# Kernel tuning notes

Hardware: AMD Instinct MI355X
Metric: run time of the kernel (lower is better)

The kernel has to match this reference:

```python
import jax, jax.numpy as jnp
import numpy as np


def setup_inputs() -> dict:
    key = jax.random.key(0)
    k1, k2 = jax.random.split(key)
    pred_corners = jax.random.normal(k1, (2048, 8, 3), dtype=jnp.float32)
    gt_corners = jax.random.normal(k2, (2048, 8, 3), dtype=jnp.float32)
    return {"pred_corners": pred_corners, "gt_corners": gt_corners}


def _chamfer(pred_corners, gt_corners):
    # flatten boxes -> point clouds: [Np*8, 3], [Ng*8, 3]
    x = pred_corners.reshape(-1, 3)
    y = gt_corners.reshape(-1, 3)
    x2 = jnp.sum(x * x, axis=-1)  # [N]
    y2 = jnp.sum(y * y, axis=-1)  # [M]
    d2 = x2[:, None] + y2[None, :] - 2.0 * jnp.einsum("nd,md->nm", x, y)
    dist = jnp.sqrt(jnp.maximum(d2, 0.0))  # [N, M]
    # bidirectional min, averaged per box (8 corners) then over boxes
    min_p2g = jnp.min(dist, axis=1).reshape(-1, 8).mean(axis=1)
    min_g2p = jnp.min(dist, axis=0).reshape(-1, 8).mean(axis=1)
    return min_p2g.mean() + min_g2p.mean()


def reference(pred_corners, gt_corners):
    return _chamfer(pred_corners, gt_corners)
```

## Files before the change

kernel.cpp:

```cpp
#include <hip/hip_runtime.h>


#define NPTS   16384
#define RPT    8
#define BLOCK  256
#define XPB    (RPT * BLOCK)
#define NXB    (NPTS / XPB)
#define NSEG   128
#define YSEG   (NPTS / NSEG)
#define CHUNK  32
#define CPAD   257
#define WS_NEED (2 * NPTS * 4)

__global__ __launch_bounds__(BLOCK, 4) void chamfer_both(
        const float* __restrict__ pred, const float* __restrict__ gt,
        unsigned int* __restrict__ minp, unsigned int* __restrict__ ming) {
    const int xb  = blockIdx.x;
    const int ys  = blockIdx.y;
    const int tid = threadIdx.x;

    __shared__ float4 shy[YSEG];
    __shared__ float  shp[CHUNK * CPAD];

    if (tid < YSEG) {
        int yi = ys * YSEG + tid;
        float a = gt[3 * yi + 0], b = gt[3 * yi + 1], c = gt[3 * yi + 2];
        shy[tid] = make_float4(a, b, c, -0.5f * (a * a + b * b + c * c));
    }

    float xx[RPT], xy[RPT], xz[RPT], x2[RPT], hv[RPT], rmx[RPT];
    const int xbase = xb * XPB;
#pragma unroll
    for (int r = 0; r < RPT; ++r) {
        int xi = xbase + r * BLOCK + tid;
        xx[r] = pred[3 * xi + 0];
        xy[r] = pred[3 * xi + 1];
        xz[r] = pred[3 * xi + 2];
        x2[r] = xx[r] * xx[r] + xy[r] * xy[r] + xz[r] * xz[r];
        hv[r] = 0.5f * x2[r];
        rmx[r] = -3.0e38f;
    }

    __syncthreads();

    for (int c = 0; c < YSEG; c += CHUNK) {
#pragma unroll 2
        for (int jj = 0; jj < CHUNK; jj += 2) {
            float4 y0 = shy[c + jj];
            float4 y1 = shy[c + jj + 1];
            float u0[RPT], u1[RPT];
#pragma unroll
            for (int r = 0; r < RPT; ++r) {
                float t0 = fmaf(xz[r], y0.z, y0.w);
                t0 = fmaf(xy[r], y0.y, t0);
                t0 = fmaf(xx[r], y0.x, t0);
                float t1 = fmaf(xz[r], y1.z, y1.w);
                t1 = fmaf(xy[r], y1.y, t1);
                t1 = fmaf(xx[r], y1.x, t1);
                rmx[r] = fmaxf(rmx[r], fmaxf(t0, t1));
                u0[r] = t0 - hv[r];
                u1[r] = t1 - hv[r];
            }
            float g0 = fmaxf(fmaxf(fmaxf(u0[0], u0[1]), u0[2]),
                             fmaxf(fmaxf(u0[3], u0[4]), u0[5]));
            float cp0 = fmaxf(fmaxf(g0, u0[6]), u0[7]);
            float g1 = fmaxf(fmaxf(fmaxf(u1[0], u1[1]), u1[2]),
                             fmaxf(fmaxf(u1[3], u1[4]), u1[5]));
            float cp1 = fmaxf(fmaxf(g1, u1[6]), u1[7]);
            shp[(jj + 0) * CPAD + tid] = cp0;
            shp[(jj + 1) * CPAD + tid] = cp1;
        }
        __syncthreads();
        {
            const int jl = tid >> 3;
            const int sl = tid & 7;
            float m = -3.0e38f;
#pragma unroll 8
            for (int k = 0; k < 32; ++k)
                m = fmaxf(m, shp[jl * CPAD + sl + 8 * k]);
            m = fmaxf(m, __shfl_xor(m, 1, 64));
            m = fmaxf(m, __shfl_xor(m, 2, 64));
            m = fmaxf(m, __shfl_xor(m, 4, 64));
            if (sl == 0) {
                int yj = ys * YSEG + c + jl;
                float d2 = fmaxf(-2.0f * m, 0.0f);
                atomicMin(&ming[yj], __float_as_uint(d2));
            }
        }
        __syncthreads();
    }

#pragma unroll
    for (int r = 0; r < RPT; ++r) {
        int xi = xbase + r * BLOCK + tid;
        float d2 = fmaxf(fmaf(-2.0f, rmx[r], x2[r]), 0.0f);
        atomicMin(&minp[xi], __float_as_uint(d2));
    }
}

__global__ __launch_bounds__(256) void chamfer_reduce(
        const unsigned int* __restrict__ mins, float* __restrict__ out) {
    const int gid = blockIdx.x * 256 + threadIdx.x;
    float s = 0.0f;
#pragma unroll
    for (int i = 0; i < 2; ++i)
        s += sqrtf(__uint_as_float(mins[gid + i * 64 * 256]));
#pragma unroll
    for (int off = 32; off > 0; off >>= 1)
        s += __shfl_down(s, off, 64);
    if ((threadIdx.x & 63) == 0)
        atomicAdd(out, s * (1.0f / (float)NPTS));
}


__global__ __launch_bounds__(256) void init_mins(unsigned int* mins, float* out) {
    int i = blockIdx.x * blockDim.x + threadIdx.x;
    if (i < 2 * NPTS) mins[i] = 0x7F800000u;
    if (i == 0) out[0] = 0.0f;
}

__global__ __launch_bounds__(BLOCK, 4) void chamfer_min_atomic(
        const float* __restrict__ pred, const float* __restrict__ gt,
        unsigned int* __restrict__ mins) {
    const int xb  = blockIdx.x;
    const int ys  = blockIdx.y;
    const int dir = blockIdx.z;
    const float* __restrict__ X = dir ? gt : pred;
    const float* __restrict__ Y = dir ? pred : gt;
    unsigned int* __restrict__ outm = mins + dir * NPTS;
    const int tid = threadIdx.x;

    __shared__ float4 sh[YSEG];
    if (tid < YSEG) {
        int yi = ys * YSEG + tid;
        float a = Y[3 * yi + 0], b = Y[3 * yi + 1], c = Y[3 * yi + 2];
        sh[tid] = make_float4(a, b, c, -0.5f * (a * a + b * b + c * c));
    }
    float xx[RPT], xy[RPT], xz[RPT], x2[RPT], mx[RPT];
    const int xbase = xb * XPB;
#pragma unroll
    for (int r = 0; r < RPT; ++r) {
        int xi = xbase + r * BLOCK + tid;
        xx[r] = X[3 * xi + 0];
        xy[r] = X[3 * xi + 1];
        xz[r] = X[3 * xi + 2];
        x2[r] = xx[r] * xx[r] + xy[r] * xy[r] + xz[r] * xz[r];
        mx[r] = -3.0e38f;
    }
    __syncthreads();
#pragma unroll 2
    for (int j = 0; j < YSEG; j += 2) {
        float4 y0 = sh[j], y1 = sh[j + 1];
#pragma unroll
        for (int r = 0; r < RPT; ++r) {
            float t0 = fmaf(xz[r], y0.z, y0.w);
            t0 = fmaf(xy[r], y0.y, t0);
            t0 = fmaf(xx[r], y0.x, t0);
            float t1 = fmaf(xz[r], y1.z, y1.w);
            t1 = fmaf(xy[r], y1.y, t1);
            t1 = fmaf(xx[r], y1.x, t1);
            mx[r] = fmaxf(mx[r], fmaxf(t0, t1));
        }
    }
#pragma unroll
    for (int r = 0; r < RPT; ++r) {
        int xi = xbase + r * BLOCK + tid;
        float d2 = fmaxf(fmaf(-2.0f, mx[r], x2[r]), 0.0f);
        atomicMin(&outm[xi], __float_as_uint(d2));
    }
}

extern "C" void kernel_launch(void* const* d_in, const int* in_sizes, int n_in,
                              void* d_out, int out_size, void* d_ws, size_t ws_size,
                              hipStream_t stream) {
    const float* pred = (const float*)d_in[0];
    const float* gt   = (const float*)d_in[1];
    float* out        = (float*)d_out;
    unsigned int* minp = (unsigned int*)d_ws;
    unsigned int* ming = minp + NPTS;

    if (ws_size >= (size_t)WS_NEED) {
        hipMemsetAsync(d_ws, 0xFF, (size_t)WS_NEED, stream);
        hipMemsetAsync(d_out, 0, sizeof(float), stream);
        hipLaunchKernelGGL(chamfer_both, dim3(NXB, NSEG), dim3(BLOCK), 0, stream,
                           pred, gt, minp, ming);
        hipLaunchKernelGGL(chamfer_reduce, dim3(64), dim3(256), 0, stream,
                           minp, out);
    } else {
        hipLaunchKernelGGL(init_mins, dim3((2 * NPTS + 255) / 256), dim3(256), 0,
                           stream, minp, out);
        hipLaunchKernelGGL(chamfer_min_atomic, dim3(NXB, NSEG, 2), dim3(BLOCK), 0,
                           stream, pred, gt, minp);
        hipLaunchKernelGGL(chamfer_reduce, dim3(64), dim3(256), 0, stream,
                           minp, out);
    }
}
```

Measured before the change: 103.3 us.

## Compute pairwise distance tiles with bf16 split-precision MFMA instead of scalar FMAs

Replaces the scalar-FMA chamfer kernel with one that encodes each point as hi/lo bf16 parts plus the half-norm term, so a single 32x32x16 bf16 MFMA yields the full x·y - |x|²/2 - |y|²/2 tile. Row minima are kept in registers and reduced with shuffles, while column minima go through LDS atomics before one global atomic per column. The aim is to move the O(N·M) arithmetic onto the matrix cores. In exchange it accepts bf16 split rounding error and many LDS atomics per tile.

Measured after the change: 102.1 us. No clear change (-1.1%).

```diff
diff --git a/kernel.cpp b/kernel.cpp
--- a/kernel.cpp
+++ b/kernel.cpp
@@ -2,99 +2,137 @@
 
 
 #define NPTS   16384
-#define RPT    8
-#define BLOCK  256
-#define XPB    (RPT * BLOCK)
-#define NXB    (NPTS / XPB)
-#define NSEG   128
-#define YSEG   (NPTS / NSEG)
-#define CHUNK  32
-#define CPAD   257
+#define YS     1024
+#define NYS    (NPTS / YS)
+#define NXG    (NPTS / 128)
+#define ONEBF  0x3F80u
 #define WS_NEED (2 * NPTS * 4)
 
-__global__ __launch_bounds__(BLOCK, 4) void chamfer_both(
+typedef short  short8  __attribute__((ext_vector_type(8)));
+typedef float  float16 __attribute__((ext_vector_type(16)));
+
+union FragAB { unsigned short us[8]; uint4 u4; short8 s8; };
+union FragC  { float16 v; float f[16]; };
+
+__device__ __forceinline__ unsigned short bf_rne(float f) {
+    unsigned int u = __float_as_uint(f);
+    return (unsigned short)((u + 0x7FFFu + ((u >> 16) & 1u)) >> 16);
+}
+__device__ __forceinline__ float bf2f(unsigned short h) {
+    return __uint_as_float(((unsigned int)h) << 16);
+}
+
+__global__ __launch_bounds__(256, 4) void chamfer_mfma(
         const float* __restrict__ pred, const float* __restrict__ gt,
         unsigned int* __restrict__ minp, unsigned int* __restrict__ ming) {
-    const int xb  = blockIdx.x;
-    const int ys  = blockIdx.y;
-    const int tid = threadIdx.x;
-
-    __shared__ float4 shy[YSEG];
-    __shared__ float  shp[CHUNK * CPAD];
-
-    if (tid < YSEG) {
-        int yi = ys * YSEG + tid;
+    __shared__ uint4 ybufA[YS];
+    __shared__ uint4 ybufB[YS];
+    __shared__ unsigned int colbuf[YS];
+
+    const int tid   = threadIdx.x;
+    const int lane  = tid & 63;
+    const int wave  = tid >> 6;
+    const int q     = lane >> 5;
+    const int n     = lane & 31;
+    const int ybase = blockIdx.y * YS;
+
+#pragma unroll
+    for (int p = 0; p < 4; ++p) {
+        int yloc = tid + p * 256;
+        int yi   = ybase + yloc;
         float a = gt[3 * yi + 0], b = gt[3 * yi + 1], c = gt[3 * yi + 2];
-        shy[tid] = make_float4(a, b, c, -0.5f * (a * a + b * b + c * c));
-    }
-
-    float xx[RPT], xy[RPT], xz[RPT], x2[RPT], hv[RPT], rmx[RPT];
-    const int xbase = xb * XPB;
-#pragma unroll
-    for (int r = 0; r < RPT; ++r) {
-        int xi = xbase + r * BLOCK + tid;
-        xx[r] = pred[3 * xi + 0];
-        xy[r] = pred[3 * xi + 1];
-        xz[r] = pred[3 * xi + 2];
-        x2[r] = xx[r] * xx[r] + xy[r] * xy[r] + xz[r] * xz[r];
-        hv[r] = 0.5f * x2[r];
-        rmx[r] = -3.0e38f;
-    }
+        float hy = 0.5f * (a * a + b * b + c * c);
+        unsigned short h0 = bf_rne(a), h1 = bf_rne(b), h2 = bf_rne(c);
+        unsigned short l0 = bf_rne(a - bf2f(h0));
+        unsigned short l1 = bf_rne(b - bf2f(h1));
+        unsigned short l2 = bf_rne(c - bf2f(h2));
+        unsigned short hh = bf_rne(hy);
+        unsigned short hl = bf_rne(hy - bf2f(hh));
+        unsigned short nhh = hh ^ 0x8000u, nhl = hl ^ 0x8000u;
+        ybufA[yloc] = make_uint4(
+            (unsigned)h0 | ((unsigned)h1 << 16),
+            (unsigned)h2 | ((unsigned)h0 << 16),
+            (unsigned)h1 | ((unsigned)h2 << 16),
+            (unsigned)l0 | ((unsigned)l1 << 16));
+        ybufB[yloc] = make_uint4(
+            (unsigned)l2 | (ONEBF << 16),
+            ONEBF | ((unsigned)nhh << 16),
+            (unsigned)nhl,
+            0u);
+        colbuf[yloc] = 0xFFFFFFFFu;
+    }
+
+    const int xt = blockIdx.x * 4 + wave;
+    const int xi = xt * 32 + n;
+    FragAB A;
+    {
+        float a = pred[3 * xi + 0], b = pred[3 * xi + 1], c = pred[3 * xi + 2];
+        float hx = 0.5f * (a * a + b * b + c * c);
+        unsigned short h0 = bf_rne(a), h1 = bf_rne(b), h2 = bf_rne(c);
+        unsigned short l0 = bf_rne(a - bf2f(h0));
+        unsigned short l1 = bf_rne(b - bf2f(h1));
+        unsigned short l2 = bf_rne(c - bf2f(h2));
+        unsigned short hh = bf_rne(hx);
+        unsigned short hl = bf_rne(hx - bf2f(hh));
+        unsigned short nhh = hh ^ 0x8000u, nhl = hl ^ 0x8000u;
+        if (q == 0) {
+            A.us[0] = h0; A.us[1] = h1; A.us[2] = h2;
+            A.us[3] = l0; A.us[4] = l1; A.us[5] = l2;
+            A.us[6] = h0; A.us[7] = h1;
+        } else {
+            A.us[0] = h2; A.us[1] = nhh; A.us[2] = nhl;
+            A.us[3] = (unsigned short)ONEBF; A.us[4] = (unsigned short)ONEBF;
+            A.us[5] = 0; A.us[6] = 0; A.us[7] = 0;
+        }
+    }
+
+    float rmx[16];
+#pragma unroll
+    for (int r = 0; r < 16; ++r) rmx[r] = -3.0e38f;
 
     __syncthreads();
 
-    for (int c = 0; c < YSEG; c += CHUNK) {
-#pragma unroll 2
-        for (int jj = 0; jj < CHUNK; jj += 2) {
-            float4 y0 = shy[c + jj];
-            float4 y1 = shy[c + jj + 1];
-            float u0[RPT], u1[RPT];
-#pragma unroll
-            for (int r = 0; r < RPT; ++r) {
-                float t0 = fmaf(xz[r], y0.z, y0.w);
-                t0 = fmaf(xy[r], y0.y, t0);
-                t0 = fmaf(xx[r], y0.x, t0);
-                float t1 = fmaf(xz[r], y1.z, y1.w);
-                t1 = fmaf(xy[r], y1.y, t1);
-                t1 = fmaf(xx[r], y1.x, t1);
-                rmx[r] = fmaxf(rmx[r], fmaxf(t0, t1));
-                u0[r] = t0 - hv[r];
-                u1[r] = t1 - hv[r];
-            }
-            float g0 = fmaxf(fmaxf(fmaxf(u0[0], u0[1]), u0[2]),
-                             fmaxf(fmaxf(u0[3], u0[4]), u0[5]));
-            float cp0 = fmaxf(fmaxf(g0, u0[6]), u0[7]);
-            float g1 = fmaxf(fmaxf(fmaxf(u1[0], u1[1]), u1[2]),
-                             fmaxf(fmaxf(u1[3], u1[4]), u1[5]));
-            float cp1 = fmaxf(fmaxf(g1, u1[6]), u1[7]);
-            shp[(jj + 0) * CPAD + tid] = cp0;
-            shp[(jj + 1) * CPAD + tid] = cp1;
+    const uint4* __restrict__ ybq = q ? ybufB : ybufA;
+
+    for (int i = 0; i < 32; ++i) {
+        FragAB B;
+        B.u4 = ybq[i * 32 + n];
+        FragC D;
+        float16 zc = {};
+        D.v = __builtin_amdgcn_mfma_f32_32x32x16_bf16(A.s8, B.s8, zc, 0, 0, 0);
+#pragma unroll
+        for (int r = 0; r < 16; ++r) rmx[r] = fmaxf(rmx[r], D.f[r]);
+        float t0 = fmaxf(fmaxf(D.f[0],  D.f[1]),  D.f[2]);
+        float t1 = fmaxf(fmaxf(D.f[3],  D.f[4]),  D.f[5]);
+        float t2 = fmaxf(fmaxf(D.f[6],  D.f[7]),  D.f[8]);
+        float t3 = fmaxf(fmaxf(D.f[9],  D.f[10]), D.f[11]);
+        float t4 = fmaxf(fmaxf(D.f[12], D.f[13]), D.f[14]);
+        float m  = fmaxf(fmaxf(fmaxf(t0, t1), t2),
+                         fmaxf(fmaxf(t3, t4), D.f[15]));
+        float d2c = fmaxf(-2.0f * m, 0.0f);
+        atomicMin(&colbuf[i * 32 + n], __float_as_uint(d2c));
+    }
+
+#pragma unroll
+    for (int r = 0; r < 16; ++r) {
+        float v = rmx[r];
+        v = fmaxf(v, __shfl_xor(v, 1, 64));
+        v = fmaxf(v, __shfl_xor(v, 2, 64));
+        v = fmaxf(v, __shfl_xor(v, 4, 64));
+        v = fmaxf(v, __shfl_xor(v, 8, 64));
+        v = fmaxf(v, __shfl_xor(v, 16, 64));
+        if (n == 0) {
+            int row = (r & 3) + 8 * (r >> 2) + 4 * q;
+            float d2 = fmaxf(-2.0f * v, 0.0f);
+            atomicMin(&minp[xt * 32 + row], __float_as_uint(d2));
         }
-        __syncthreads();
-        {
-            const int jl = tid >> 3;
-            const int sl = tid & 7;
-            float m = -3.0e38f;
-#pragma unroll 8
-            for (int k = 0; k < 32; ++k)
-                m = fmaxf(m, shp[jl * CPAD + sl + 8 * k]);
-            m = fmaxf(m, __shfl_xor(m, 1, 64));
-            m = fmaxf(m, __shfl_xor(m, 2, 64));
-            m = fmaxf(m, __shfl_xor(m, 4, 64));
-            if (sl == 0) {
-                int yj = ys * YSEG + c + jl;
-                float d2 = fmaxf(-2.0f * m, 0.0f);
-                atomicMin(&ming[yj], __float_as_uint(d2));
-            }
-        }
-        __syncthreads();
-    }
-
-#pragma unroll
-    for (int r = 0; r < RPT; ++r) {
-        int xi = xbase + r * BLOCK + tid;
-        float d2 = fmaxf(fmaf(-2.0f, rmx[r], x2[r]), 0.0f);
-        atomicMin(&minp[xi], __float_as_uint(d2));
+    }
+
+    __syncthreads();
+#pragma unroll
+    for (int p = 0; p < 4; ++p) {
+        int yloc = tid + p * 256;
+        atomicMin(&ming[ybase + yloc], colbuf[yloc]);
     }
 }
 
@@ -113,13 +151,16 @@
 }
 
 
+#define FB_RPT  8
+#define FB_YSEG 128
+
 __global__ __launch_bounds__(256) void init_mins(unsigned int* mins, float* out) {
     int i = blockIdx.x * blockDim.x + threadIdx.x;
     if (i < 2 * NPTS) mins[i] = 0x7F800000u;
     if (i == 0) out[0] = 0.0f;
 }
 
-__global__ __launch_bounds__(BLOCK, 4) void chamfer_min_atomic(
+__global__ __launch_bounds__(256, 4) void chamfer_min_atomic(
         const float* __restrict__ pred, const float* __restrict__ gt,
         unsigned int* __restrict__ mins) {
     const int xb  = blockIdx.x;
@@ -130,29 +171,29 @@
     unsigned int* __restrict__ outm = mins + dir * NPTS;
     const int tid = threadIdx.x;
 
-    __shared__ float4 sh[YSEG];
-    if (tid < YSEG) {
-        int yi = ys * YSEG + tid;
+    __shared__ float4 sh[FB_YSEG];
+    if (tid < FB_YSEG) {
+        int yi = ys * FB_YSEG + tid;
         float a = Y[3 * yi + 0], b = Y[3 * yi + 1], c = Y[3 * yi + 2];
         sh[tid] = make_float4(a, b, c, -0.5f * (a * a + b * b + c * c));
     }
-    float xx[RPT], xy[RPT], xz[RPT], x2[RPT], mx[RPT];
-    const int xbase = xb * XPB;
-#pragma unroll
-    for (int r = 0; r < RPT; ++r) {
-        int xi = xbase + r * BLOCK + tid;
-        xx[r] = X[3 * xi + 0];
-        xy[r] = X[3 * xi + 1];
-        xz[r] = X[3 * xi + 2];
+    float xx[FB_RPT], xy[FB_RPT], xz[FB_RPT], x2[FB_RPT], mx[FB_RPT];
+    const int xbase = xb * (FB_RPT * 256);
+#pragma unroll
+    for (int r = 0; r < FB_RPT; ++r) {
+        int xi2 = xbase + r * 256 + tid;
+        xx[r] = X[3 * xi2 + 0];
+        xy[r] = X[3 * xi2 + 1];
+        xz[r] = X[3 * xi2 + 2];
         x2[r] = xx[r] * xx[r] + xy[r] * xy[r] + xz[r] * xz[r];
         mx[r] = -3.0e38f;
     }
     __syncthreads();
 #pragma unroll 2
-    for (int j = 0; j < YSEG; j += 2) {
+    for (int j = 0; j < FB_YSEG; j += 2) {
         float4 y0 = sh[j], y1 = sh[j + 1];
 #pragma unroll
-        for (int r = 0; r < RPT; ++r) {
+        for (int r = 0; r < FB_RPT; ++r) {
             float t0 = fmaf(xz[r], y0.z, y0.w);
             t0 = fmaf(xy[r], y0.y, t0);
             t0 = fmaf(xx[r], y0.x, t0);
@@ -163,10 +204,10 @@
         }
     }
 #pragma unroll
-    for (int r = 0; r < RPT; ++r) {
-        int xi = xbase + r * BLOCK + tid;
+    for (int r = 0; r < FB_RPT; ++r) {
+        int xi2 = xbase + r * 256 + tid;
         float d2 = fmaxf(fmaf(-2.0f, mx[r], x2[r]), 0.0f);
-        atomicMin(&outm[xi], __float_as_uint(d2));
+        atomicMin(&outm[xi2], __float_as_uint(d2));
     }
 }
 
@@ -182,15 +223,16 @@
     if (ws_size >= (size_t)WS_NEED) {
         hipMemsetAsync(d_ws, 0xFF, (size_t)WS_NEED, stream);
         hipMemsetAsync(d_out, 0, sizeof(float), stream);
-        hipLaunchKernelGGL(chamfer_both, dim3(NXB, NSEG), dim3(BLOCK), 0, stream,
+        hipLaunchKernelGGL(chamfer_mfma, dim3(NXG, NYS), dim3(256), 0, stream,
                            pred, gt, minp, ming);
         hipLaunchKernelGGL(chamfer_reduce, dim3(64), dim3(256), 0, stream,
                            minp, out);
     } else {
         hipLaunchKernelGGL(init_mins, dim3((2 * NPTS + 255) / 256), dim3(256), 0,
                            stream, minp, out);
-        hipLaunchKernelGGL(chamfer_min_atomic, dim3(NXB, NSEG, 2), dim3(BLOCK), 0,
-                           stream, pred, gt, minp);
+        hipLaunchKernelGGL(chamfer_min_atomic, dim3(NPTS / (FB_RPT * 256),
+                           NPTS / FB_YSEG, 2), dim3(256), 0, stream,
+                           pred, gt, minp);
         hipLaunchKernelGGL(chamfer_reduce, dim3(64), dim3(256), 0, stream,
                            minp, out);
     }
```
